# Kernel tuning notes

Measured on AMD Instinct MI355X. Metric: run time of the kernel, lower is better.

## Reference

```python
import jax, jax.numpy as jnp
import numpy as np

B, C, H, W = 8, 128, 64, 64
KC = 32  # key_channels

def setup_inputs() -> dict:
    key = jax.random.key(0)
    ks = jax.random.split(key, 6)
    s = lambda fan_in: 1.0 / np.sqrt(fan_in)
    x  = jax.random.normal(ks[0], (B, C, H, W), dtype=jnp.float32)
    Wq = jax.random.uniform(ks[1], (KC, C), jnp.float32, -s(C), s(C))  # 1x1 conv kernels
    Wk = jax.random.uniform(ks[2], (KC, C), jnp.float32, -s(C), s(C))
    Wv = jax.random.uniform(ks[3], (C, C), jnp.float32, -s(C), s(C))
    Wo = jax.random.uniform(ks[4], (C, C), jnp.float32, -s(C), s(C))
    gamma = jnp.zeros((1,), jnp.float32) + 0.1  # nonzero so attention path matters
    return {"x": x, "Wq": Wq, "Wk": Wk, "Wv": Wv, "Wo": Wo, "gamma": gamma}

def reference(x, Wq, Wk, Wv, Wo, gamma):
    b, c, h, w = x.shape
    xf = x.reshape(b, c, h * w)                      # [B,C,N]
    Q = jnp.einsum('qc,bcn->bnq', Wq, xf)            # [B,N,KC]
    K = jnp.einsum('kc,bcn->bkn', Wk, xf)            # [B,KC,N]
    V = jnp.einsum('vc,bcn->bnv', Wv, xf)            # [B,N,C]
    scores = jnp.einsum('bnq,bqm->bnm', Q, K) / jnp.sqrt(jnp.asarray(Wq.shape[0], x.dtype))
    attn = jax.nn.softmax(scores, axis=-1)           # [B,N,N]
    out = jnp.einsum('bnm,bmv->bvn', attn, V)        # [B,C,N]
    out = jnp.einsum('oc,bcn->bon', Wo, out).reshape(b, c, h, w)
    return x + gamma * out
```

## Files before the change

### kernel.cpp

```cpp
#include <hip/hip_runtime.h>
#include <hip/hip_bf16.h>

#define BB 8
#define CC 128
#define NN 4096
#define KCQ 32

typedef unsigned short u16;
typedef unsigned int u32;
typedef unsigned char u8;
typedef __bf16 bf16x8 __attribute__((ext_vector_type(8)));
typedef float f32x4 __attribute__((ext_vector_type(4)));
typedef long i64;

typedef const __attribute__((address_space(1))) void gas_t;
typedef __attribute__((address_space(3))) void las_t;

__device__ __forceinline__ u16 f2bf(float f){
  u32 u = __builtin_bit_cast(u32, f);
  u32 r = u + 0x7FFFu + ((u >> 16) & 1u);
  return (u16)(r >> 16);
}
__device__ __forceinline__ u32 cvtpk(float lo, float hi){
  u32 r; asm("v_cvt_pk_bf16_f32 %0, %1, %2" : "=v"(r) : "v"(lo), "v"(hi)); return r;
}
__device__ __forceinline__ u32 pk_fp8x4(float a, float b, float c, float d){
  int v = 0;
  v = __builtin_amdgcn_cvt_pk_fp8_f32(a, b, v, false);
  v = __builtin_amdgcn_cvt_pk_fp8_f32(c, d, v, true);
  return (u32)v;
}
__device__ __forceinline__ void gload16(const void* g, void* l){
  __builtin_amdgcn_global_load_lds((gas_t*)g, (las_t*)l, 16, 0, 0);
}

__global__ __launch_bounds__(256) void k_prep_w(const float* Wq, const float* Wk,
                                                const float* Wv, const float* Wo,
                                                u16* wsq, u16* wsk, u16* wsv, u16* wso){
  int i = blockIdx.x * 256 + threadIdx.x;
  const float SC = 0.2550350f;
  if (i < 4096)       wsq[i]        = f2bf(Wq[i] * SC);
  else if (i < 8192)  wsk[i-4096]   = f2bf(Wk[i-4096]);
  else if (i < 24576) wsv[i-8192]   = f2bf(Wv[i-8192]);
  else if (i < 40960) wso[i-24576]  = f2bf(Wo[i-24576]);
}

__global__ __launch_bounds__(512) void k_projx(const float* x, const u16* wq, const u16* wk,
                                               const u16* wv, u16* Qm, u16* Km, u8* Vt8){
  __shared__ __align__(16) u16 xL[64*132];
  int b = blockIdx.x >> 6, nb = (blockIdx.x & 63) * 64;
  int t = threadIdx.x;
  int n = t & 63, cg = t >> 6;
  #pragma unroll
  for (int it = 0; it < 16; ++it){
    int c = it*8 + cg;
    xL[n*132 + c] = f2bf(x[((size_t)b*CC + c)*NN + nb + n]);
  }
  __syncthreads();
  int w = t >> 6, l = t & 63, a = l & 15, g = l >> 4;
  int ns = w >> 1, half = w & 1;
  int n0 = nb + ns*16;
  bf16x8 xa[4];
  #pragma unroll
  for (int kc = 0; kc < 4; ++kc)
    xa[kc] = *(const bf16x8*)(xL + (ns*16 + a)*132 + kc*32 + g*8);
  __syncthreads();

  u32* vbuf = (u32*)xL;
  auto Vjob = [&](int vt){
    f32x4 acc = {0.f,0.f,0.f,0.f};
    #pragma unroll
    for (int kc = 0; kc < 4; ++kc){
      bf16x8 wa = ((const bf16x8*)(wv + (size_t)(vt*16 + a) * CC))[kc*4 + g];
      acc = __builtin_amdgcn_mfma_f32_16x16x32_bf16(xa[kc], wa, acc, 0,0,0);
    }
    int row = vt*16 + a;
    vbuf[row*16 + ((ns ^ ((a>>1)&3)) << 2) + g] = pk_fp8x4(acc[0], acc[1], acc[2], acc[3]);
  };

  if (half == 0){
    #pragma unroll
    for (int qt = 0; qt < 2; ++qt){
      f32x4 accq = {0.f,0.f,0.f,0.f}, acck = {0.f,0.f,0.f,0.f};
      #pragma unroll
      for (int kc = 0; kc < 4; ++kc){
        bf16x8 wbq = ((const bf16x8*)(wq + (size_t)(qt*16 + a) * CC))[kc*4 + g];
        bf16x8 wbk = ((const bf16x8*)(wk + (size_t)(qt*16 + a) * CC))[kc*4 + g];
        accq = __builtin_amdgcn_mfma_f32_16x16x32_bf16(xa[kc], wbq, accq, 0,0,0);
        acck = __builtin_amdgcn_mfma_f32_16x16x32_bf16(xa[kc], wbk, acck, 0,0,0);
      }
      #pragma unroll
      for (int r = 0; r < 4; ++r){
        Qm[((size_t)b*NN + n0 + 4*g + r) * KCQ + qt*16 + a] = f2bf(accq[r]);
        Km[((size_t)b*NN + n0 + 4*g + r) * KCQ + qt*16 + a] = f2bf(acck[r]);
      }
    }
    Vjob(0); Vjob(1);
  } else {
    #pragma unroll
    for (int vt = 2; vt < 8; ++vt) Vjob(vt);
  }
  __syncthreads();
  {
    int row = t >> 2, ck = t & 3, key = (row >> 1) & 3;
    uint4 d = ((const uint4*)vbuf)[row*4 + (ck ^ key)];
    *(uint4*)(Vt8 + ((size_t)b*CC + row)*NN + nb + ck*16) = d;
  }
}

__global__ __launch_bounds__(512, 4) void k_attn(const u16* Qm, const u16* Km,
                                                 const u8* Vt8, const u16* wso,
                                                 const float* x, const float* gamma,
                                                 float* out){
  __shared__ __align__(16) char smem[65536];
  int bid = blockIdx.x;
  int b = bid & 7, qb = bid >> 3;
  int t0 = threadIdx.x;
  int l = t0 & 63, a = l & 15, g = l >> 4;
  int w = t0 >> 6, h = w >> 2, wq = w & 3;
  int q0 = qb * 64;
  int kb0 = h * 2048;

  const u8* Vb = Vt8 + (size_t)b * CC * NN;

  bf16x8 qf[4];
  #pragma unroll
  for (int qs = 0; qs < 4; ++qs)
    qf[qs] = ((const bf16x8*)(Qm + ((size_t)b*NN + q0 + qs*16 + a) * KCQ))[g];
  const u16* kPtr = Km + ((size_t)b*NN + kb0 + wq*16 + a) * KCQ + g*8;

  f32x4 o[8];
  #pragma unroll
  for (int i = 0; i < 8; ++i) o[i] = (f32x4){0.f,0.f,0.f,0.f};
  float ls[4] = {0.f, 0.f, 0.f, 0.f};

  int schk = (l&3) ^ ((l>>3)&3);
  const u8* vSrc = Vb + (size_t)(wq*32 + (l>>2))*NN + kb0 + (schk << 4);
  const int vOff = h*8192 + wq*2048 + l*16;
  auto stageV = [&](int t1, int sl){
    const u8* vs = vSrc + t1*64;
    char* vd = smem + sl*16384 + vOff;
    gload16(vs, vd);
    gload16(vs + (size_t)16*NN, vd + 1024);
  };

  const int cswz = (a >> 1) & 3;
  auto PV = [&](int ps, int vsl){
    const char* Vs = smem + vsl*16384 + h*8192;
    const char* Pr = smem + 49152 + ps*8192 + h*4096;
    __builtin_amdgcn_s_setprio(1);
    #pragma unroll
    for (int kk = 0; kk < 2; ++kk){
      int kx = (((kk*2 + (g>>1)) ^ cswz) << 4) + (g&1)*8;
      i64 vf0 = *(const i64*)(Vs + (wq*32 + a)*64 + kx);
      i64 vf1 = *(const i64*)(Vs + (wq*32 + 16 + a)*64 + kx);
      i64 pf[4];
      #pragma unroll
      for (int qs = 0; qs < 4; ++qs)
        pf[qs] = *(const i64*)(Pr + (qs*16 + a)*64 + kx);
      #pragma unroll
      for (int qs = 0; qs < 4; ++qs){
        o[qs*2  ] = __builtin_amdgcn_mfma_f32_16x16x32_fp8_fp8(vf0, pf[qs], o[qs*2  ], 0,0,0);
        o[qs*2+1] = __builtin_amdgcn_mfma_f32_16x16x32_fp8_fp8(vf1, pf[qs], o[qs*2+1], 0,0,0);
      }
    }
    __builtin_amdgcn_s_setprio(0);
  };

  auto SM = [&](const f32x4* sv, char* Pw){
    #pragma unroll
    for (int qs = 0; qs < 4; ++qs){
      float p0 = __builtin_amdgcn_exp2f(sv[qs][0]);
      float p1 = __builtin_amdgcn_exp2f(sv[qs][1]);
      float p2 = __builtin_amdgcn_exp2f(sv[qs][2]);
      float p3 = __builtin_amdgcn_exp2f(sv[qs][3]);
      ls[qs] += (p0 + p1) + (p2 + p3);
      *(u32*)(Pw + (qs*16 + a)*64 + ((wq ^ cswz) << 4) + 4*g) = pk_fp8x4(p0, p1, p2, p3);
    }
  };

  char* PwBase = smem + 49152 + h*4096;

  bf16x8 kfC = *(const bf16x8*)(kPtr);
  bf16x8 kfN = *(const bf16x8*)(kPtr + 2048);
  stageV(0, 0);
  stageV(1, 1);
  {
    f32x4 sv[4];
    #pragma unroll
    for (int qs = 0; qs < 4; ++qs){
      f32x4 z = {0.f,0.f,0.f,0.f};
      sv[qs] = __builtin_amdgcn_mfma_f32_16x16x32_bf16(kfC, qf[qs], z, 0,0,0);
    }
    SM(sv, PwBase);
  }
  asm volatile("s_waitcnt vmcnt(2) lgkmcnt(0)" ::: "memory");
  __builtin_amdgcn_s_barrier();

  int vR = 0;
  for (int t = 0; t < 31; ++t){
    f32x4 sv[4];
    #pragma unroll
    for (int qs = 0; qs < 4; ++qs){
      f32x4 z = {0.f,0.f,0.f,0.f};
      sv[qs] = __builtin_amdgcn_mfma_f32_16x16x32_bf16(kfN, qf[qs], z, 0,0,0);
    }
    PV(t & 1, vR);
    SM(sv, PwBase + ((t+1)&1)*8192);
    if (t < 30){
      kfC = *(const bf16x8*)(kPtr + (size_t)(t+2)*2048);
      int sl = vR >= 1 ? vR - 1 : 2;
      stageV(t+2, sl);
      asm volatile("s_waitcnt vmcnt(3) lgkmcnt(0)" ::: "memory");
    } else {
      asm volatile("s_waitcnt vmcnt(0) lgkmcnt(0)" ::: "memory");
    }
    __builtin_amdgcn_s_barrier();
    kfN = kfC;
    vR = (vR == 2) ? 0 : vR + 1;
  }
  PV(1, vR);

  #pragma unroll
  for (int qs = 0; qs < 4; ++qs){
    ls[qs] += __shfl_xor(ls[qs], 16);
    ls[qs] += __shfl_xor(ls[qs], 32);
  }
  float* Ml = (float*)(smem + 36864);
  if (l < 16){
    #pragma unroll
    for (int qs = 0; qs < 4; ++qs) Ml[w*64 + qs*16 + l] = ls[qs];
  }
  float* Cx = (float*)smem;
  __syncthreads();
  if (h == 1){
    #pragma unroll
    for (int i = 0; i < 8; ++i){
      int qs = i >> 1, st = i & 1;
      *(f32x4*)(Cx + (qs*16 + a)*132 + wq*32 + st*16 + 4*g) = o[i];
    }
  }
  __syncthreads();
  u16* Ol = (u16*)(smem + 49152);
  if (h == 0){
    #pragma unroll
    for (int qs = 0; qs < 4; ++qs){
      float lsum = 0.f;
      #pragma unroll
      for (int ww = 0; ww < 8; ++ww) lsum += Ml[ww*64 + qs*16 + a];
      float inv = 1.f / lsum;
      #pragma unroll
      for (int st = 0; st < 2; ++st){
        f32x4 oc = o[qs*2 + st];
        const float* cx = Cx + (qs*16 + a)*132 + wq*32 + st*16 + 4*g;
        uint2 pk;
        pk.x = cvtpk((oc[0] + cx[0]) * inv, (oc[1] + cx[1]) * inv);
        pk.y = cvtpk((oc[2] + cx[2]) * inv, (oc[3] + cx[3]) * inv);
        int chunk = (wq*4 + st*2 + (g>>1)) ^ (a & 7);
        *(uint2*)((char*)Ol + (qs*16 + a)*256 + chunk*16 + (g&1)*8) = pk;
      }
    }
  }
  __syncthreads();
  float gm = gamma[0];
  f32x4 acc2[4];
  #pragma unroll
  for (int qs = 0; qs < 4; ++qs) acc2[qs] = (f32x4){0.f,0.f,0.f,0.f};
  #pragma unroll
  for (int kc = 0; kc < 4; ++kc){
    bf16x8 wof = *(const bf16x8*)(wso + (size_t)(w*16 + a)*CC + kc*32 + g*8);
    #pragma unroll
    for (int qs = 0; qs < 4; ++qs){
      int chunk = (kc*4 + g) ^ (a & 7);
      bf16x8 of = *(const bf16x8*)((const char*)Ol + (qs*16 + a)*256 + chunk*16);
      acc2[qs] = __builtin_amdgcn_mfma_f32_16x16x32_bf16(wof, of, acc2[qs], 0,0,0);
    }
  }
  #pragma unroll
  for (int qs = 0; qs < 4; ++qs){
    #pragma unroll
    for (int r = 0; r < 4; ++r){
      size_t idx = ((size_t)b*CC + w*16 + 4*g + r)*NN + q0 + qs*16 + a;
      out[idx] = x[idx] + gm * acc2[qs][r];
    }
  }
}

extern "C" void kernel_launch(void* const* d_in, const int* in_sizes, int n_in,
                              void* d_out, int out_size, void* d_ws, size_t ws_size,
                              hipStream_t stream) {
  const float* x     = (const float*)d_in[0];
  const float* Wq    = (const float*)d_in[1];
  const float* Wk    = (const float*)d_in[2];
  const float* Wv    = (const float*)d_in[3];
  const float* Wo    = (const float*)d_in[4];
  const float* gamma = (const float*)d_in[5];
  float* out = (float*)d_out;

  u16* wsq = (u16*)d_ws;
  u16* wsk = wsq + 4096;
  u16* wsv = wsk + 4096;
  u16* wso = wsv + 16384;
  u16* Qm  = wso + 16384;
  u16* Km  = Qm + (size_t)BB*NN*KCQ;
  u8*  Vt8 = (u8*)(Km + (size_t)BB*NN*KCQ);

  hipLaunchKernelGGL(k_prep_w, dim3(160), dim3(256), 0, stream, Wq, Wk, Wv, Wo, wsq, wsk, wsv, wso);
  hipLaunchKernelGGL(k_projx,  dim3(512), dim3(512), 0, stream, x, wsq, wsk, wsv, Qm, Km, Vt8);
  hipLaunchKernelGGL(k_attn,   dim3(512), dim3(512), 0, stream, Qm, Km, Vt8, wso, x, gamma, out);
}
```

Before: 71.42 us.

## Widen attention query tile to 128 and split waves by value channels instead of keys

The attention kernel now handles 128 queries per block with 256 blocks instead of 64 queries with 512 blocks. Waves now divide the work by value channels and query halves rather than by two key halves, so the cross-half output reduction through shared memory goes away. The V tile is reorganised to 128-key rows and double-buffered. The projection kernel's V transpose write is changed to an interleaved byte order that matches the new fp8 MFMA operand layout. In exchange, register pressure rises (8 Q fragments and 8 score tiles), the launch bound occupancy hint drops to 2, and every iteration now waits for all loads to finish (vmcnt(0)), which reduces the overlap between loads and compute.

```diff
diff --git a/kernel.cpp b/kernel.cpp
--- a/kernel.cpp
+++ b/kernel.cpp
@@ -12,6 +12,7 @@
 typedef __bf16 bf16x8 __attribute__((ext_vector_type(8)));
 typedef float f32x4 __attribute__((ext_vector_type(4)));
 typedef long i64;
+typedef long i64x2 __attribute__((ext_vector_type(2)));
 
 typedef const __attribute__((address_space(1))) void gas_t;
 typedef __attribute__((address_space(3))) void las_t;
@@ -102,13 +103,17 @@
   }
   __syncthreads();
   {
-    int row = t >> 2, ck = t & 3, key = (row >> 1) & 3;
-    uint4 d = ((const uint4*)vbuf)[row*4 + (ck ^ key)];
-    *(uint4*)(Vt8 + ((size_t)b*CC + row)*NN + nb + ck*16) = d;
-  }
-}
-
-__global__ __launch_bounds__(512, 4) void k_attn(const u16* Qm, const u16* Km,
+    int row = t >> 2, gg = t & 3, key = (row >> 1) & 3;
+    const u32* vb = vbuf + row*16;
+    auto rd = [&](int d){ return vb[(((d>>2)^key)<<2) + (d&3)]; };
+    uint4 dd;
+    dd.x = rd(2*gg);     dd.y = rd(2*gg+1);
+    dd.z = rd(8+2*gg);   dd.w = rd(9+2*gg);
+    *(uint4*)(Vt8 + ((size_t)b*CC + row)*NN + nb + gg*16) = dd;
+  }
+}
+
+__global__ __launch_bounds__(512, 2) void k_attn(const u16* Qm, const u16* Km,
                                                  const u8* Vt8, const u16* wso,
                                                  const float* x, const float* gamma,
                                                  float* out){
@@ -117,173 +122,168 @@
   int b = bid & 7, qb = bid >> 3;
   int t0 = threadIdx.x;
   int l = t0 & 63, a = l & 15, g = l >> 4;
-  int w = t0 >> 6, h = w >> 2, wq = w & 3;
-  int q0 = qb * 64;
-  int kb0 = h * 2048;
+  int w = t0 >> 6;
+  int q0 = qb * 128;
+  int qh = (w >> 2) * 64;
+  int vch0 = (w & 3) * 32;
 
   const u8* Vb = Vt8 + (size_t)b * CC * NN;
 
-  bf16x8 qf[4];
-  #pragma unroll
-  for (int qs = 0; qs < 4; ++qs)
+  bf16x8 qf[8];
+  #pragma unroll
+  for (int qs = 0; qs < 8; ++qs)
     qf[qs] = ((const bf16x8*)(Qm + ((size_t)b*NN + q0 + qs*16 + a) * KCQ))[g];
-  const u16* kPtr = Km + ((size_t)b*NN + kb0 + wq*16 + a) * KCQ + g*8;
+
+  const u16* kPtr = Km + ((size_t)b*NN + w*16 + a) * KCQ + g*8;
 
   f32x4 o[8];
   #pragma unroll
   for (int i = 0; i < 8; ++i) o[i] = (f32x4){0.f,0.f,0.f,0.f};
-  float ls[4] = {0.f, 0.f, 0.f, 0.f};
-
-  int schk = (l&3) ^ ((l>>3)&3);
-  const u8* vSrc = Vb + (size_t)(wq*32 + (l>>2))*NN + kb0 + (schk << 4);
-  const int vOff = h*8192 + wq*2048 + l*16;
-  auto stageV = [&](int t1, int sl){
-    const u8* vs = vSrc + t1*64;
-    char* vd = smem + sl*16384 + vOff;
-    gload16(vs, vd);
-    gload16(vs + (size_t)16*NN, vd + 1024);
+  float ls[8] = {0.f,0.f,0.f,0.f,0.f,0.f,0.f,0.f};
+
+  int csrc = ((l&7) ^ (l>>3)) << 4;
+  const u8* vS0 = Vb + (size_t)(w*16 +     (l>>3))*NN + csrc;
+  const u8* vS1 = Vb + (size_t)(w*16 + 8 + (l>>3))*NN + csrc;
+  const int vD0 = w*2048 + l*16;
+  const int vD1 = w*2048 + 1024 + l*16;
+  auto stageV = [&](int kt1, int sl){
+    char* base = smem + sl*16384;
+    gload16(vS0 + kt1*128, base + vD0);
+    gload16(vS1 + kt1*128, base + vD1);
   };
 
-  const int cswz = (a >> 1) & 3;
-  auto PV = [&](int ps, int vsl){
-    const char* Vs = smem + vsl*16384 + h*8192;
-    const char* Pr = smem + 49152 + ps*8192 + h*4096;
-    __builtin_amdgcn_s_setprio(1);
-    #pragma unroll
-    for (int kk = 0; kk < 2; ++kk){
-      int kx = (((kk*2 + (g>>1)) ^ cswz) << 4) + (g&1)*8;
-      i64 vf0 = *(const i64*)(Vs + (wq*32 + a)*64 + kx);
-      i64 vf1 = *(const i64*)(Vs + (wq*32 + 16 + a)*64 + kx);
-      i64 pf[4];
-      #pragma unroll
-      for (int qs = 0; qs < 4; ++qs)
-        pf[qs] = *(const i64*)(Pr + (qs*16 + a)*64 + kx);
-      #pragma unroll
-      for (int qs = 0; qs < 4; ++qs){
-        o[qs*2  ] = __builtin_amdgcn_mfma_f32_16x16x32_fp8_fp8(vf0, pf[qs], o[qs*2  ], 0,0,0);
-        o[qs*2+1] = __builtin_amdgcn_mfma_f32_16x16x32_fp8_fp8(vf1, pf[qs], o[qs*2+1], 0,0,0);
-      }
-    }
-    __builtin_amdgcn_s_setprio(0);
-  };
+  int pbase = ((w>>2)&1)*64 + ((((w&1)<<1) | (g>>1)))*16 + ((w>>1)&1)*8 + (g&1)*4;
+  const int pswz = (((pbase >> 4) ^ (a&7)) << 4) | (pbase & 15);
 
   auto SM = [&](const f32x4* sv, char* Pw){
     #pragma unroll
-    for (int qs = 0; qs < 4; ++qs){
+    for (int qs = 0; qs < 8; ++qs){
       float p0 = __builtin_amdgcn_exp2f(sv[qs][0]);
       float p1 = __builtin_amdgcn_exp2f(sv[qs][1]);
       float p2 = __builtin_amdgcn_exp2f(sv[qs][2]);
       float p3 = __builtin_amdgcn_exp2f(sv[qs][3]);
       ls[qs] += (p0 + p1) + (p2 + p3);
-      *(u32*)(Pw + (qs*16 + a)*64 + ((wq ^ cswz) << 4) + 4*g) = pk_fp8x4(p0, p1, p2, p3);
+      *(u32*)(Pw + (qs*16 + a)*128 + pswz) = pk_fp8x4(p0, p1, p2, p3);
     }
   };
 
-  char* PwBase = smem + 49152 + h*4096;
-
-  bf16x8 kfC = *(const bf16x8*)(kPtr);
-  bf16x8 kfN = *(const bf16x8*)(kPtr + 2048);
+  auto PV = [&](int sl){
+    const char* Vs = smem + sl*16384;
+    const char* Pr = smem + 32768 + sl*16384;
+    __builtin_amdgcn_s_setprio(1);
+    i64x2 vf[2][2];
+    #pragma unroll
+    for (int sub = 0; sub < 2; ++sub)
+      #pragma unroll
+      for (int p = 0; p < 2; ++p)
+        vf[sub][p] = *(const i64x2*)(Vs + (vch0 + sub*16 + a)*128 + (((p*4+g) ^ (a&7))<<4));
+    #pragma unroll
+    for (int qs = 0; qs < 4; ++qs){
+      #pragma unroll
+      for (int p = 0; p < 2; ++p){
+        i64x2 pf = *(const i64x2*)(Pr + (qh + qs*16 + a)*128 + (((p*4+g) ^ (a&7))<<4));
+        o[qs]   = __builtin_amdgcn_mfma_f32_16x16x32_fp8_fp8(vf[0][p][0], pf[0], o[qs],   0,0,0);
+        o[qs]   = __builtin_amdgcn_mfma_f32_16x16x32_fp8_fp8(vf[0][p][1], pf[1], o[qs],   0,0,0);
+        o[4+qs] = __builtin_amdgcn_mfma_f32_16x16x32_fp8_fp8(vf[1][p][0], pf[0], o[4+qs], 0,0,0);
+        o[4+qs] = __builtin_amdgcn_mfma_f32_16x16x32_fp8_fp8(vf[1][p][1], pf[1], o[4+qs], 0,0,0);
+      }
+    }
+    __builtin_amdgcn_s_setprio(0);
+  };
+
+  char* P0 = smem + 32768;
+  char* P1 = smem + 49152;
+
+  bf16x8 kfN = *(const bf16x8*)(kPtr);
+  bf16x8 kfP = *(const bf16x8*)(kPtr + 4096);
   stageV(0, 0);
-  stageV(1, 1);
   {
-    f32x4 sv[4];
-    #pragma unroll
-    for (int qs = 0; qs < 4; ++qs){
-      f32x4 z = {0.f,0.f,0.f,0.f};
-      sv[qs] = __builtin_amdgcn_mfma_f32_16x16x32_bf16(kfC, qf[qs], z, 0,0,0);
-    }
-    SM(sv, PwBase);
-  }
-  asm volatile("s_waitcnt vmcnt(2) lgkmcnt(0)" ::: "memory");
-  __builtin_amdgcn_s_barrier();
-
-  int vR = 0;
-  for (int t = 0; t < 31; ++t){
-    f32x4 sv[4];
-    #pragma unroll
-    for (int qs = 0; qs < 4; ++qs){
+    f32x4 sv[8];
+    #pragma unroll
+    for (int qs = 0; qs < 8; ++qs){
       f32x4 z = {0.f,0.f,0.f,0.f};
       sv[qs] = __builtin_amdgcn_mfma_f32_16x16x32_bf16(kfN, qf[qs], z, 0,0,0);
     }
-    PV(t & 1, vR);
-    SM(sv, PwBase + ((t+1)&1)*8192);
-    if (t < 30){
-      kfC = *(const bf16x8*)(kPtr + (size_t)(t+2)*2048);
-      int sl = vR >= 1 ? vR - 1 : 2;
-      stageV(t+2, sl);
-      asm volatile("s_waitcnt vmcnt(3) lgkmcnt(0)" ::: "memory");
-    } else {
-      asm volatile("s_waitcnt vmcnt(0) lgkmcnt(0)" ::: "memory");
-    }
+    SM(sv, P0);
+  }
+  asm volatile("s_waitcnt vmcnt(0) lgkmcnt(0)" ::: "memory");
+  __builtin_amdgcn_s_barrier();
+  kfN = kfP;
+
+  for (int t = 0; t < 31; ++t){
+    if (t < 30) kfP = *(const bf16x8*)(kPtr + (size_t)(t+2)*4096);
+    stageV(t+1, (t+1)&1);
+    f32x4 sv[8];
+    #pragma unroll
+    for (int qs = 0; qs < 8; ++qs){
+      f32x4 z = {0.f,0.f,0.f,0.f};
+      sv[qs] = __builtin_amdgcn_mfma_f32_16x16x32_bf16(kfN, qf[qs], z, 0,0,0);
+    }
+    PV(t & 1);
+    SM(sv, (t & 1) ? P0 : P1);
+    asm volatile("s_waitcnt vmcnt(0) lgkmcnt(0)" ::: "memory");
     __builtin_amdgcn_s_barrier();
-    kfN = kfC;
-    vR = (vR == 2) ? 0 : vR + 1;
-  }
-  PV(1, vR);
-
-  #pragma unroll
-  for (int qs = 0; qs < 4; ++qs){
+    kfN = kfP;
+  }
+  PV(1);
+
+  #pragma unroll
+  for (int qs = 0; qs < 8; ++qs){
     ls[qs] += __shfl_xor(ls[qs], 16);
     ls[qs] += __shfl_xor(ls[qs], 32);
   }
-  float* Ml = (float*)(smem + 36864);
+  float* Ml = (float*)smem;
   if (l < 16){
     #pragma unroll
-    for (int qs = 0; qs < 4; ++qs) Ml[w*64 + qs*16 + l] = ls[qs];
-  }
-  float* Cx = (float*)smem;
-  __syncthreads();
-  if (h == 1){
-    #pragma unroll
-    for (int i = 0; i < 8; ++i){
-      int qs = i >> 1, st = i & 1;
-      *(f32x4*)(Cx + (qs*16 + a)*132 + wq*32 + st*16 + 4*g) = o[i];
-    }
-  }
-  __syncthreads();
-  u16* Ol = (u16*)(smem + 49152);
-  if (h == 0){
+    for (int qs = 0; qs < 8; ++qs) Ml[w*128 + qs*16 + l] = ls[qs];
+  }
+  __syncthreads();
+  float inv4[4];
+  #pragma unroll
+  for (int qs = 0; qs < 4; ++qs){
+    int gq = (qh >> 4) + qs;
+    float s = 0.f;
+    #pragma unroll
+    for (int ww = 0; ww < 8; ++ww) s += Ml[ww*128 + gq*16 + a];
+    inv4[qs] = 1.f / s;
+  }
+  __syncthreads();
+  u16* Ol = (u16*)smem;
+  #pragma unroll
+  for (int sub = 0; sub < 2; ++sub)
     #pragma unroll
     for (int qs = 0; qs < 4; ++qs){
-      float lsum = 0.f;
-      #pragma unroll
-      for (int ww = 0; ww < 8; ++ww) lsum += Ml[ww*64 + qs*16 + a];
-      float inv = 1.f / lsum;
-      #pragma unroll
-      for (int st = 0; st < 2; ++st){
-        f32x4 oc = o[qs*2 + st];
-        const float* cx = Cx + (qs*16 + a)*132 + wq*32 + st*16 + 4*g;
-        uint2 pk;
-        pk.x = cvtpk((oc[0] + cx[0]) * inv, (oc[1] + cx[1]) * inv);
-        pk.y = cvtpk((oc[2] + cx[2]) * inv, (oc[3] + cx[3]) * inv);
-        int chunk = (wq*4 + st*2 + (g>>1)) ^ (a & 7);
-        *(uint2*)((char*)Ol + (qs*16 + a)*256 + chunk*16 + (g&1)*8) = pk;
-      }
-    }
-  }
+      f32x4 oc = o[sub*4 + qs];
+      float iv = inv4[qs];
+      uint2 pk;
+      pk.x = cvtpk(oc[0]*iv, oc[1]*iv);
+      pk.y = cvtpk(oc[2]*iv, oc[3]*iv);
+      int qrow = qh + qs*16 + a;
+      int chunk = ((w&3)*4 + sub*2 + (g>>1)) ^ (a&7);
+      *(uint2*)((char*)Ol + qrow*256 + chunk*16 + (g&1)*8) = pk;
+    }
   __syncthreads();
   float gm = gamma[0];
-  f32x4 acc2[4];
-  #pragma unroll
-  for (int qs = 0; qs < 4; ++qs) acc2[qs] = (f32x4){0.f,0.f,0.f,0.f};
+  f32x4 acc2[8];
+  #pragma unroll
+  for (int i = 0; i < 8; ++i) acc2[i] = (f32x4){0.f,0.f,0.f,0.f};
   #pragma unroll
   for (int kc = 0; kc < 4; ++kc){
     bf16x8 wof = *(const bf16x8*)(wso + (size_t)(w*16 + a)*CC + kc*32 + g*8);
     #pragma unroll
-    for (int qs = 0; qs < 4; ++qs){
+    for (int qs = 0; qs < 8; ++qs){
       int chunk = (kc*4 + g) ^ (a & 7);
       bf16x8 of = *(const bf16x8*)((const char*)Ol + (qs*16 + a)*256 + chunk*16);
       acc2[qs] = __builtin_amdgcn_mfma_f32_16x16x32_bf16(wof, of, acc2[qs], 0,0,0);
     }
   }
   #pragma unroll
-  for (int qs = 0; qs < 4; ++qs){
+  for (int qs = 0; qs < 8; ++qs)
     #pragma unroll
     for (int r = 0; r < 4; ++r){
       size_t idx = ((size_t)b*CC + w*16 + 4*g + r)*NN + q0 + qs*16 + a;
       out[idx] = x[idx] + gm * acc2[qs][r];
     }
-  }
 }
 
 extern "C" void kernel_launch(void* const* d_in, const int* in_sizes, int n_in,
@@ -307,5 +307,5 @@
 
   hipLaunchKernelGGL(k_prep_w, dim3(160), dim3(256), 0, stream, Wq, Wk, Wv, Wo, wsq, wsk, wsv, wso);
   hipLaunchKernelGGL(k_projx,  dim3(512), dim3(512), 0, stream, x, wsq, wsk, wsv, Qm, Km, Vt8);
-  hipLaunchKernelGGL(k_attn,   dim3(512), dim3(512), 0, stream, Qm, Km, Vt8, wso, x, gamma, out);
-}
+  hipLaunchKernelGGL(k_attn,   dim3(256), dim3(512), 0, stream, Qm, Km, Vt8, wso, x, gamma, out);
+}
```

Result: slower. 74.50 us (+4.3%).

## Permute fp8 K-dimension layout of V and P so PV uses 128-bit LDS reads

Applied to the files above, without the earlier changes.

Changes the key ordering inside each 64-key tile, both in the V transpose written by the projection kernel and in the P tile written by softmax. Each lane then reads its two MFMA K-chunks with a single 16-byte LDS load instead of two 8-byte loads. This halves the LDS load instructions in the PV inner loop. The cost is extra scalar 32-bit LDS reads when assembling V rows in the projection kernel, and the two permutations must match exactly for the result to stay correct.

```diff
diff --git a/kernel.cpp b/kernel.cpp
--- a/kernel.cpp
+++ b/kernel.cpp
@@ -12,6 +12,7 @@
 typedef __bf16 bf16x8 __attribute__((ext_vector_type(8)));
 typedef float f32x4 __attribute__((ext_vector_type(4)));
 typedef long i64;
+typedef long i64x2 __attribute__((ext_vector_type(2)));
 
 typedef const __attribute__((address_space(1))) void gas_t;
 typedef __attribute__((address_space(3))) void las_t;
@@ -102,9 +103,13 @@
   }
   __syncthreads();
   {
-    int row = t >> 2, ck = t & 3, key = (row >> 1) & 3;
-    uint4 d = ((const uint4*)vbuf)[row*4 + (ck ^ key)];
-    *(uint4*)(Vt8 + ((size_t)b*CC + row)*NN + nb + ck*16) = d;
+    int row = t >> 2, gg = t & 3, key = (row >> 1) & 3;
+    const u32* vb = vbuf + row*16;
+    auto rd = [&](int d){ return vb[(((d>>2)^key)<<2) + (d&3)]; };
+    uint4 dd;
+    dd.x = rd(2*gg);     dd.y = rd(2*gg+1);
+    dd.z = rd(8+2*gg);   dd.w = rd(9+2*gg);
+    *(uint4*)(Vt8 + ((size_t)b*CC + row)*NN + nb + gg*16) = dd;
   }
 }
 
@@ -145,28 +150,25 @@
   };
 
   const int cswz = (a >> 1) & 3;
+  const int rc = (g ^ cswz) << 4;
   auto PV = [&](int ps, int vsl){
     const char* Vs = smem + vsl*16384 + h*8192;
     const char* Pr = smem + 49152 + ps*8192 + h*4096;
     __builtin_amdgcn_s_setprio(1);
-    #pragma unroll
-    for (int kk = 0; kk < 2; ++kk){
-      int kx = (((kk*2 + (g>>1)) ^ cswz) << 4) + (g&1)*8;
-      i64 vf0 = *(const i64*)(Vs + (wq*32 + a)*64 + kx);
-      i64 vf1 = *(const i64*)(Vs + (wq*32 + 16 + a)*64 + kx);
-      i64 pf[4];
-      #pragma unroll
-      for (int qs = 0; qs < 4; ++qs)
-        pf[qs] = *(const i64*)(Pr + (qs*16 + a)*64 + kx);
-      #pragma unroll
-      for (int qs = 0; qs < 4; ++qs){
-        o[qs*2  ] = __builtin_amdgcn_mfma_f32_16x16x32_fp8_fp8(vf0, pf[qs], o[qs*2  ], 0,0,0);
-        o[qs*2+1] = __builtin_amdgcn_mfma_f32_16x16x32_fp8_fp8(vf1, pf[qs], o[qs*2+1], 0,0,0);
-      }
+    i64x2 vf0 = *(const i64x2*)(Vs + (wq*32 + a)*64 + rc);
+    i64x2 vf1 = *(const i64x2*)(Vs + (wq*32 + 16 + a)*64 + rc);
+    #pragma unroll
+    for (int qs = 0; qs < 4; ++qs){
+      i64x2 pf = *(const i64x2*)(Pr + (qs*16 + a)*64 + rc);
+      o[qs*2  ] = __builtin_amdgcn_mfma_f32_16x16x32_fp8_fp8(vf0[0], pf[0], o[qs*2  ], 0,0,0);
+      o[qs*2  ] = __builtin_amdgcn_mfma_f32_16x16x32_fp8_fp8(vf0[1], pf[1], o[qs*2  ], 0,0,0);
+      o[qs*2+1] = __builtin_amdgcn_mfma_f32_16x16x32_fp8_fp8(vf1[0], pf[0], o[qs*2+1], 0,0,0);
+      o[qs*2+1] = __builtin_amdgcn_mfma_f32_16x16x32_fp8_fp8(vf1[1], pf[1], o[qs*2+1], 0,0,0);
     }
     __builtin_amdgcn_s_setprio(0);
   };
 
+  const int ppos = (((((wq&1)<<1) | (g>>1)) ^ cswz) << 4) | ((wq>>1) << 3) | ((g&1) << 2);
   auto SM = [&](const f32x4* sv, char* Pw){
     #pragma unroll
     for (int qs = 0; qs < 4; ++qs){
@@ -175,7 +177,7 @@
       float p2 = __builtin_amdgcn_exp2f(sv[qs][2]);
       float p3 = __builtin_amdgcn_exp2f(sv[qs][3]);
       ls[qs] += (p0 + p1) + (p2 + p3);
-      *(u32*)(Pw + (qs*16 + a)*64 + ((wq ^ cswz) << 4) + 4*g) = pk_fp8x4(p0, p1, p2, p3);
+      *(u32*)(Pw + (qs*16 + a)*64 + ppos) = pk_fp8x4(p0, p1, p2, p3);
     }
   };
 
```

Result: faster. 68.70 us (-3.8%).
